# Kernel optimization log

Hardware: AMD Instinct MI355X
Metric: run time of the kernel (lower is better)

## Reference

```python
import jax, jax.numpy as jnp
import numpy as np

D_MODEL, N_HEADS, N_AGENTS = 1024, 16, 64
HEAD_DIM = D_MODEL // N_HEADS
B, N = 4, 4096


def setup_inputs() -> dict:
    key = jax.random.key(0)
    ks = jax.random.split(key, 12)
    hs = HEAD_DIM
    inp = {
        "q": jax.random.normal(ks[0], (B, N_HEADS, N, hs), jnp.float32),
        "k": jax.random.normal(ks[1], (B, N_HEADS, N, hs), jnp.float32),
        "v": jax.random.normal(ks[2], (B, N_HEADS, N, hs), jnp.float32),
        # per-head linear layers (torch nn.Linear: y = x @ W.T + b)
        "Wq": jax.random.normal(ks[3], (hs, hs), jnp.float32) / np.sqrt(hs),
        "bq": jnp.zeros((hs,), jnp.float32),
        "Wk": jax.random.normal(ks[4], (hs, hs), jnp.float32) / np.sqrt(hs),
        "bk": jnp.zeros((hs,), jnp.float32),
        "Wv": jax.random.normal(ks[5], (hs, hs), jnp.float32) / np.sqrt(hs),
        "bv": jnp.zeros((hs,), jnp.float32),
        "Wo": jax.random.normal(ks[6], (D_MODEL, D_MODEL), jnp.float32) / np.sqrt(D_MODEL),
        "bo": jnp.zeros((D_MODEL,), jnp.float32),
        "agent_tokens": jax.random.normal(ks[7], (1, N_HEADS, N_AGENTS, hs), jnp.float32),
    }
    return inp


def reference(q, k, v, Wq, bq, Wk, bk, Wv, bv, Wo, bo, agent_tokens):
    Bq, nh, N_, hs = q.shape
    scale = 1.0 / np.sqrt(hs).astype(np.float32)
    agents = jnp.broadcast_to(agent_tokens, (Bq, nh, N_AGENTS, hs))
    q_agents = jnp.einsum("bhad,ed->bhae", agents, Wq) + bq   # [B,nh,A,hs]
    k_agents = jnp.einsum("bhnd,ed->bhne", k, Wk) + bk        # [B,nh,N,hs]
    v_agents = jnp.einsum("bhnd,ed->bhne", v, Wv) + bv        # [B,nh,N,hs]
    # stage 1: agents attend to keys/values
    scores1 = jnp.einsum("bhad,bhnd->bhan", q_agents, k_agents) * scale
    scores1 = jax.nn.softmax(scores1, axis=-1)
    context1 = jnp.einsum("bhan,bhnd->bhad", scores1, v_agents)  # [B,nh,A,hs]
    # stage 2: queries attend to agent context
    scores2 = jnp.einsum("bhnd,bhad->bhna", q, context1) * scale
    scores2 = jax.nn.softmax(scores2, axis=-1)
    context2 = jnp.einsum("bhna,bhad->bhnd", scores2, context1)  # [B,nh,N,hs]
    context2 = context2.transpose(0, 2, 1, 3).reshape(Bq, N_, nh * hs)
    output = context2 @ Wo.T + bo  # dropout is identity in eval
    return output, scores2
```

## Files before the change

### kernel.cpp

```cpp
#include <hip/hip_runtime.h>

#define NB 4
#define NH 16
#define NN 4096
#define HS 64
#define NA 64
#define DM 1024
#define NBH (NB*NH)
#define SCALE 0.125f

typedef __attribute__((ext_vector_type(8))) short bf16x8;
typedef __attribute__((ext_vector_type(4))) float f32x4;

__device__ __forceinline__ unsigned short f2bf(float f) {
  unsigned u = __float_as_uint(f);
  u += 0x7FFF + ((u >> 16) & 1);
  return (unsigned short)(u >> 16);
}

__device__ __forceinline__ void gload_lds16(const void* g, void* l) {
  __builtin_amdgcn_global_load_lds(
      (const __attribute__((address_space(1))) unsigned int*)g,
      (__attribute__((address_space(3))) unsigned int*)l, 16, 0, 0);
}

__device__ __forceinline__ void fma44(float (&c)[4][4], const float4 a, const float4 b) {
  const float av[4] = {a.x, a.y, a.z, a.w};
  const float bw[4] = {b.x, b.y, b.z, b.w};
#pragma unroll
  for (int i = 0; i < 4; ++i)
#pragma unroll
    for (int j = 0; j < 4; ++j)
      c[i][j] = fmaf(av[i], bw[j], c[i][j]);
}

__device__ __forceinline__ void dot44(float (&c)[4][4], const float4 (&a)[4], const float4 (&b)[4]) {
#pragma unroll
  for (int i = 0; i < 4; ++i)
#pragma unroll
    for (int j = 0; j < 4; ++j) {
      c[i][j] = fmaf(a[i].x, b[j].x, c[i][j]);
      c[i][j] = fmaf(a[i].y, b[j].y, c[i][j]);
      c[i][j] = fmaf(a[i].z, b[j].z, c[i][j]);
      c[i][j] = fmaf(a[i].w, b[j].w, c[i][j]);
    }
}

__global__ __launch_bounds__(256) void k0_fold(
    const float* __restrict__ agents, const float* __restrict__ Wq,
    const float* __restrict__ bq, const float* __restrict__ Wk,
    unsigned short* __restrict__ foldqbf) {
  const int h = blockIdx.x, tid = threadIdx.x;
  const int tn = tid & 15, tm = tid >> 4;
  __shared__ float AG[64][68];
  __shared__ float WB[64][68];
  __shared__ float QA[64][68];
  __shared__ float WKT[64][68];
  for (int i = tid; i < 1024; i += 256) {
    const int r = i >> 4, c4 = (i & 15) * 4;
    *(float4*)&AG[r][c4] = *(const float4*)(agents + h * 4096 + r * 64 + c4);
    *(float4*)&WB[r][c4] = *(const float4*)(Wq + r * 64 + c4);
    const float4 f = *(const float4*)(Wk + r * 64 + c4);
    WKT[c4 + 0][r] = f.x; WKT[c4 + 1][r] = f.y;
    WKT[c4 + 2][r] = f.z; WKT[c4 + 3][r] = f.w;
  }
  __syncthreads();
  {
    const float4 bb = *(const float4*)(bq + tn * 4);
    float acc[4][4];
#pragma unroll
    for (int i = 0; i < 4; ++i) {
      acc[i][0] = bb.x; acc[i][1] = bb.y; acc[i][2] = bb.z; acc[i][3] = bb.w;
    }
    for (int d4 = 0; d4 < 64; d4 += 4) {
      float4 a4[4], b4[4];
#pragma unroll
      for (int i = 0; i < 4; ++i) a4[i] = *(const float4*)&AG[tm * 4 + i][d4];
#pragma unroll
      for (int j = 0; j < 4; ++j) b4[j] = *(const float4*)&WB[tn * 4 + j][d4];
      dot44(acc, a4, b4);
    }
#pragma unroll
    for (int i = 0; i < 4; ++i)
      *(float4*)&QA[tm * 4 + i][tn * 4] =
          make_float4(acc[i][0], acc[i][1], acc[i][2], acc[i][3]);
  }
// ... 76 lines not shown
        kreg[i0] = *(const float4*)(kraw + kvbase + (size_t)(t + 1) * 4096 + (size_t)i * 4);
        vreg[i0] = *(const float4*)(vraw + kvbase + (size_t)(t + 1) * 4096 + (size_t)i * 4);
      }
    }
    __syncthreads();
    const bf16x8 af0 = *(const bf16x8*)&KN[(w * 16 + l15) * 72 + lg * 8];
    const bf16x8 af1 = *(const bf16x8*)&KN[(w * 16 + l15) * 72 + 32 + lg * 8];
    f32x4 sacc[4];
#pragma unroll
    for (int afr = 0; afr < 4; ++afr) {
      sacc[afr] = (f32x4){0.f, 0.f, 0.f, 0.f};
      const bf16x8 b0 = *(const bf16x8*)&FQ[(afr * 16 + l15) * 72 + lg * 8];
      const bf16x8 b1 = *(const bf16x8*)&FQ[(afr * 16 + l15) * 72 + 32 + lg * 8];
      sacc[afr] = __builtin_amdgcn_mfma_f32_16x16x32_bf16(af0, b0, sacc[afr], 0, 0, 0);
      sacc[afr] = __builtin_amdgcn_mfma_f32_16x16x32_bf16(af1, b1, sacc[afr], 0, 0, 0);
    }
#pragma unroll
    for (int afr = 0; afr < 4; ++afr) {
      const unsigned e0 = f2bf(__expf(sacc[afr][0])) | ((unsigned)f2bf(__expf(sacc[afr][1])) << 16);
      const unsigned e1 = f2bf(__expf(sacc[afr][2])) | ((unsigned)f2bf(__expf(sacc[afr][3])) << 16);
      *(uint2*)&ES[(afr * 16 + l15) * 72 + w * 16 + lg * 4] = make_uint2(e0, e1);
    }
    __syncthreads();
    const bf16x8 ea0 = *(const bf16x8*)&ES[(w * 16 + l15) * 72 + lg * 8];
    const bf16x8 ea1 = *(const bf16x8*)&ES[(w * 16 + l15) * 72 + 32 + lg * 8];
    pacc = __builtin_amdgcn_mfma_f32_16x16x32_bf16(ea0, ones, pacc, 0, 0, 0);
    pacc = __builtin_amdgcn_mfma_f32_16x16x32_bf16(ea1, ones, pacc, 0, 0, 0);
#pragma unroll
    for (int df = 0; df < 4; ++df) {
      const int d = df * 16 + l15;
      const int sw = 8 * ((d >> 2) & 7);
      const bf16x8 vb0 = *(const bf16x8*)&VT[d * 72 + ((lg * 8) ^ sw)];
      const bf16x8 vb1 = *(const bf16x8*)&VT[d * 72 + ((32 + lg * 8) ^ sw)];
      ctx[df] = __builtin_amdgcn_mfma_f32_16x16x32_bf16(ea0, vb0, ctx[df], 0, 0, 0);
      ctx[df] = __builtin_amdgcn_mfma_f32_16x16x32_bf16(ea1, vb1, ctx[df], 0, 0, 0);
    }
  }
  const size_t pbase = ((size_t)bh * 16 + chunk) * 4096;
#pragma unroll
  for (int df = 0; df < 4; ++df)
#pragma unroll
    for (int r = 0; r < 4; ++r)
      pctx[pbase + (w * 16 + lg * 4 + r) * 64 + df * 16 + l15] = ctx[df][r];
  if (l15 == 0) {
#pragma unroll
    for (int r = 0; r < 4; ++r)
      psum[((size_t)bh * 16 + chunk) * 64 + w * 16 + lg * 4 + r] = pacc[r];
  }
}

__global__ __launch_bounds__(256) void k3_reduce(
    const float* __restrict__ pctx, const float* __restrict__ psum,
    const float* __restrict__ Wv, const float* __restrict__ bv,
    float* __restrict__ c1n) {
  const int bh = blockIdx.x, tid = threadIdx.x;
  const int tn = tid & 15, tm = tid >> 4;
  __shared__ float sinv[64];
  __shared__ float CT[64][68];
  __shared__ float WT[64][68];
  if (tid < 64) {
    float s = 0.f;
    for (int c = 0; c < 16; ++c) s += psum[((size_t)bh * 16 + c) * 64 + tid];
    sinv[tid] = 1.0f / s;
  }
  for (int i = tid; i < 1024; i += 256) {
    const int e = i >> 4, d4 = (i & 15) * 4;
    const float4 f = *(const float4*)(Wv + e * 64 + d4);
    WT[d4 + 0][e] = f.x; WT[d4 + 1][e] = f.y;
    WT[d4 + 2][e] = f.z; WT[d4 + 3][e] = f.w;
  }
  __syncthreads();
  for (int i4 = tid; i4 < 1024; i4 += 256) {
    const int a = i4 >> 4, d4 = (i4 & 15) * 4;
    float4 s = make_float4(0.f, 0.f, 0.f, 0.f);
    for (int c = 0; c < 16; ++c) {
      const float4 f = *(const float4*)(pctx + ((size_t)bh * 16 + c) * 4096 + a * 64 + d4);
      s.x += f.x; s.y += f.y; s.z += f.z; s.w += f.w;
    }
    const float si = sinv[a];
    CT[d4 + 0][a] = s.x * si; CT[d4 + 1][a] = s.y * si;
    CT[d4 + 2][a] = s.z * si; CT[d4 + 3][a] = s.w * si;
  }
  __syncthreads();
  float acc[4][4];
  const float4 bb = *(const float4*)(bv + tn * 4);
#pragma unroll
  for (int i = 0; i < 4; ++i) {
    acc[i][0] = bb.x; acc[i][1] = bb.y; acc[i][2] = bb.z; acc[i][3] = bb.w;
  }
#pragma unroll 8
  for (int d = 0; d < 64; ++d) {
    const float4 av = *(const float4*)&CT[d][tm * 4];
    const float4 wv = *(const float4*)&WT[d][tn * 4];
    fma44(acc, av, wv);
  }
#pragma unroll
  for (int i = 0; i < 4; ++i)
    *(float4*)(c1n + (size_t)bh * 4096 + (tm * 4 + i) * 64 + tn * 4) =
        make_float4(acc[i][0], acc[i][1], acc[i][2], acc[i][3]);
}

__global__ __launch_bounds__(256) void kG(
    const float* __restrict__ c1n, const float* __restrict__ Wo,
    unsigned short* __restrict__ GT) {
  const int et = blockIdx.x;
  const int bh = blockIdx.y, h = bh & 15;
  const int e0 = et * 256;
  __shared__ unsigned short WoS[256 * 72];
  __shared__ unsigned short C1S[64 * 72];
  const int tid = threadIdx.x;
  const int lane = tid & 63, w = tid >> 6;
  const int l15 = lane & 15, lg = lane >> 4;
  for (int i = tid; i < 4096; i += 256) {
    const int e = i >> 4, d4 = (i & 15) * 4;
    const float4 f = *(const float4*)(Wo + (size_t)(e0 + e) * DM + h * 64 + d4);
    ushort4 o;
    o.x = f2bf(f.x); o.y = f2bf(f.y); o.z = f2bf(f.z); o.w = f2bf(f.w);
    *(ushort4*)&WoS[e * 72 + d4] = o;
  }
  for (int i = tid; i < 1024; i += 256) {
    const int a = i >> 4, d4 = (i & 15) * 4;
    const float4 f = *(const float4*)(c1n + (size_t)bh * 4096 + a * 64 + d4);
    ushort4 o;
    o.x = f2bf(f.x); o.y = f2bf(f.y); o.z = f2bf(f.z); o.w = f2bf(f.w);
    *(ushort4*)&C1S[a * 72 + d4] = o;
  }
  __syncthreads();
  bf16x8 b0[4], b1[4];
#pragma unroll
  for (int at = 0; at < 4; ++at) {
    b0[at] = *(const bf16x8*)&C1S[(at * 16 + l15) * 72 + lg * 8];
    b1[at] = *(const bf16x8*)&C1S[(at * 16 + l15) * 72 + 32 + lg * 8];
  }
#pragma unroll
  for (int et16 = 0; et16 < 4; ++et16) {
    const int erow = w * 64 + et16 * 16 + l15;
    const bf16x8 a0 = *(const bf16x8*)&WoS[erow * 72 + lg * 8];
    const bf16x8 a1 = *(const bf16x8*)&WoS[erow * 72 + 32 + lg * 8];
#pragma unroll
    for (int at = 0; at < 4; ++at) {
      f32x4 acc = (f32x4){0.f, 0.f, 0.f, 0.f};
      acc = __builtin_amdgcn_mfma_f32_16x16x32_bf16(a0, b0[at], acc, 0, 0, 0);
      acc = __builtin_amdgcn_mfma_f32_16x16x32_bf16(a1, b1[at], acc, 0, 0, 0);
      const size_t gbase =
          ((size_t)bh * 1024 + e0 + w * 64 + et16 * 16 + lg * 4) * 64 + at * 16 + l15;
#pragma unroll
      for (int r = 0; r < 4; ++r) GT[gbase + (size_t)r * 64] = f2bf(acc[r]);
    }
  }
}

__global__ __launch_bounds__(256) void k4_mfma(
    const float* __restrict__ q, const float* __restrict__ c1n,
    float* __restrict__ scores2, unsigned short* __restrict__ P2bf) {
  __shared__ unsigned short QN[64 * 72];
  __shared__ unsigned short C1N[64 * 72];
  __shared__ unsigned short PS[64 * 72];
  const int bh = blockIdx.y;
  const int n0 = blockIdx.x * 64;
  const int tid = threadIdx.x;
  const int lane = tid & 63, w = tid >> 6;
  const int l15 = lane & 15, lg = lane >> 4;

  for (int i = tid; i < 1024; i += 256) {
    const int r = i >> 4, c4 = (i & 15) * 4;
    const float4 f = *(const float4*)(q + ((size_t)bh * NN + n0 + r) * HS + c4);
    *(uint2*)&QN[r * 72 + c4] = make_uint2(
        f2bf(f.x * SCALE) | ((unsigned)f2bf(f.y * SCALE) << 16),
        f2bf(f.z * SCALE) | ((unsigned)f2bf(f.w * SCALE) << 16));
    const float4 g = *(const float4*)(c1n + (size_t)bh * 4096 + r * 64 + c4);
    *(uint2*)&C1N[r * 72 + c4] = make_uint2(
        f2bf(g.x) | ((unsigned)f2bf(g.y) << 16),
        f2bf(g.z) | ((unsigned)f2bf(g.w) << 16));
  }
  __syncthreads();
  const bf16x8 af0 = *(const bf16x8*)&QN[(w * 16 + l15) * 72 + lg * 8];
  const bf16x8 af1 = *(const bf16x8*)&QN[(w * 16 + l15) * 72 + 32 + lg * 8];
  f32x4 sacc[4];
#pragma unroll
  for (int afr = 0; afr < 4; ++afr) {
    sacc[afr] = (f32x4){0.f, 0.f, 0.f, 0.f};
    const bf16x8 b0 = *(const bf16x8*)&C1N[(afr * 16 + l15) * 72 + lg * 8];
    const bf16x8 b1 = *(const bf16x8*)&C1N[(afr * 16 + l15) * 72 + 32 + lg * 8];
    sacc[afr] = __builtin_amdgcn_mfma_f32_16x16x32_bf16(af0, b0, sacc[afr], 0, 0, 0);
    sacc[afr] = __builtin_amdgcn_mfma_f32_16x16x32_bf16(af1, b1, sacc[afr], 0, 0, 0);
  }
  float p[4][4];
#pragma unroll
  for (int r = 0; r < 4; ++r) {
    float m = fmaxf(fmaxf(sacc[0][r], sacc[1][r]), fmaxf(sacc[2][r], sacc[3][r]));
#pragma unroll
    for (int off = 1; off < 16; off <<= 1) m = fmaxf(m, __shfl_xor(m, off));
    float s = 0.f;
#pragma unroll
    for (int afr = 0; afr < 4; ++afr) {
      p[afr][r] = __expf(sacc[afr][r] - m);
      s += p[afr][r];
    }
#pragma unroll
    for (int off = 1; off < 16; off <<= 1) s += __shfl_xor(s, off);
    const float inv = 1.0f / s;
    const size_t srow = ((size_t)bh * NN + n0 + w * 16 + lg * 4 + r) * NA;
#pragma unroll
    for (int afr = 0; afr < 4; ++afr) {
      p[afr][r] *= inv;
      scores2[srow + afr * 16 + l15] = p[afr][r];
      PS[(w * 16 + lg * 4 + r) * 72 + afr * 16 + l15] = f2bf(p[afr][r]);
    }
  }
  const int prow = w * 16 + (lane >> 2);
  const int pch = (lane & 3) * 16;
  const uint4 v0 = *(const uint4*)&PS[prow * 72 + pch];
  const uint4 v1 = *(const uint4*)&PS[prow * 72 + pch + 8];
  unsigned short* gp = P2bf + ((size_t)bh * NN + n0 + prow) * NA + pch;
  *(uint4*)gp = v0;
  *(uint4*)(gp + 8) = v1;
}

__global__ __launch_bounds__(512, 1) void k5_mfma(
    const unsigned short* __restrict__ P2, const unsigned short* __restrict__ GT,
    const float* __restrict__ bo, float* __restrict__ out) {
  __shared__ unsigned short As[2][256 * 64];
  __shared__ unsigned short Bs[2][256 * 64];
  const int tid = threadIdx.x;
  const int lane = tid & 63;
  const int w = tid >> 6;
  const int wr = w >> 2, wc = w & 3;
  const int l15 = lane & 15, lg = lane >> 4;
  const int mblk = blockIdx.x;
  const int b16 = (mblk >> 4) * 16;
  const int nloc0 = (mblk & 15) * 256;
  const int e0 = blockIdx.y * 256;

  const int srow8 = lane >> 3;
  const int sslot = ((lane & 7) ^ srow8) << 4;

  f32x4 acc[8][4] = {{{0.f}}};

#define K5_STAGE(T, BUF)                                                       \
  {                                                                            \
    const char* Ab = (const char*)(P2 + ((size_t)(b16 + (T)) * NN + nloc0) * NA); \
    const char* Gb = (const char*)(GT + ((size_t)(b16 + (T)) * 1024 + e0) * NA);  \
    _Pragma("unroll")                                                          \
    for (int j = 0; j < 4; ++j) {                                              \
      const int rb = j * 64 + w * 8;                \
      const int r = rb + srow8;                                                \
      gload_lds16(Ab + (size_t)r * 128 + sslot,                                \
                  (char*)As[BUF] + rb * 128 + lane * 16);                      \
      gload_lds16(Gb + (size_t)r * 128 + sslot,                                \
                  (char*)Bs[BUF] + rb * 128 + lane * 16);                      \
    }                                                                          \
  }

  K5_STAGE(0, 0);
  K5_STAGE(1, 1);
  for (int t = 0; t < 16; ++t) {
    if (t < 15) {
      asm volatile("s_waitcnt vmcnt(8)" ::: "memory");
    } else {
      asm volatile("s_waitcnt vmcnt(0)" ::: "memory");
    }
    __builtin_amdgcn_sched_barrier(0);
    __builtin_amdgcn_s_barrier();
    __builtin_amdgcn_sched_barrier(0);
    const char* Ac = (const char*)As[t & 1];
    const char* Bc = (const char*)Bs[t & 1];
#pragma unroll
    for (int ks = 0; ks < 2; ++ks) {
      bf16x8 af[8], bfr[4];
#pragma unroll
      for (int m = 0; m < 8; ++m) {
        const int r = wr * 128 + m * 16 + l15;
        const int byt = (ks * 64 + lg * 16) ^ ((r & 7) << 4);
        af[m] = *(const bf16x8*)(Ac + r * 128 + byt);
      }
#pragma unroll
      for (int n = 0; n < 4; ++n) {
        const int r = wc * 64 + n * 16 + l15;
        const int byt = (ks * 64 + lg * 16) ^ ((r & 7) << 4);
        bfr[n] = *(const bf16x8*)(Bc + r * 128 + byt);
      }
#pragma unroll
      for (int m = 0; m < 8; ++m)
#pragma unroll
        for (int n = 0; n < 4; ++n)
          acc[m][n] = __builtin_amdgcn_mfma_f32_16x16x32_bf16(af[m], bfr[n], acc[m][n], 0, 0, 0);
    }
    __builtin_amdgcn_sched_barrier(0);
    __builtin_amdgcn_s_barrier();
    __builtin_amdgcn_sched_barrier(0);
    if (t + 2 < 16) K5_STAGE(t + 2, t & 1);
  }
#undef K5_STAGE

  const size_t mrow0 = (size_t)(b16 >> 4) * NN + nloc0;
#pragma unroll
  for (int m = 0; m < 8; ++m) {
    const size_t row0 = mrow0 + wr * 128 + m * 16 + lg * 4;
#pragma unroll
    for (int n = 0; n < 4; ++n) {
      const int c = e0 + wc * 64 + n * 16 + l15;
      const float bias = bo[c];
#pragma unroll
      for (int r = 0; r < 4; ++r)
        out[(row0 + r) * DM + c] = acc[m][n][r] + bias;
    }
  }
}

extern "C" void kernel_launch(void* const* d_in, const int* in_sizes, int n_in,
                              void* d_out, int out_size, void* d_ws, size_t ws_size,
                              hipStream_t stream) {
  (void)in_sizes; (void)n_in; (void)out_size; (void)ws_size;
  const float* q  = (const float*)d_in[0];
  const float* k  = (const float*)d_in[1];
  const float* v  = (const float*)d_in[2];
  const float* Wq = (const float*)d_in[3];
  const float* bq = (const float*)d_in[4];
  const float* Wk = (const float*)d_in[5];
  const float* bk = (const float*)d_in[6];
  const float* Wv = (const float*)d_in[7];
  const float* bv = (const float*)d_in[8];
  const float* Wo = (const float*)d_in[9];
  const float* bo = (const float*)d_in[10];
  const float* ag = (const float*)d_in[11];
  (void)bk;

  float* out0 = (float*)d_out;
  float* scores2 = out0 + (size_t)NB * NN * DM;

  float* ws = (float*)d_ws;
  unsigned short* foldqbf = (unsigned short*)ws;
  float* c1n = ws + 65536;
  float* psum = c1n + 262144;
  float* pctx = psum + 65536;
  unsigned short* GT = (unsigned short*)pctx;
  unsigned short* P2bf = (unsigned short*)(pctx + 4194304);

  k0_fold<<<NH, 256, 0, stream>>>(ag, Wq, bq, Wk, foldqbf);
  k2_mfma<<<dim3(16, NBH), 256, 0, stream>>>(k, v, foldqbf, pctx, psum);
  k3_reduce<<<NBH, 256, 0, stream>>>(pctx, psum, Wv, bv, c1n);
  kG<<<dim3(4, NBH), 256, 0, stream>>>(c1n, Wo, GT);
  k4_mfma<<<dim3(NN / 64, NBH), 256, 0, stream>>>(q, c1n, scores2, P2bf);
  k5_mfma<<<dim3(NB * NN / 256, DM / 256), 512, 0, stream>>>(P2bf, GT, bo, out0);
}
```

Measured before the change: 152.5 us.

## Interleave k5 prefetch with MFMA quadrants, swizzle blocks, split k3 reduce

The k5 GEMM main loop is restructured into four MFMA quadrants per K-step. Each quadrant loads only its own LDS fragments, interleaves one quarter of the next tile's global-to-LDS loads, and raises wave priority with s_setprio around the MFMA bursts. The block index is swizzled so neighbouring workgroups share P2/GT tiles in cache. k3_reduce is split into 4 blocks per head over the agent dimension to get more parallelism, at the cost of reloading Wv per block. The added barriers and the single-buffer-ahead prefetch risk extra sync overhead.

```diff
diff --git a/kernel.cpp b/kernel.cpp
--- a/kernel.cpp
+++ b/kernel.cpp
@@ -215,14 +215,17 @@
     const float* __restrict__ pctx, const float* __restrict__ psum,
     const float* __restrict__ Wv, const float* __restrict__ bv,
     float* __restrict__ c1n) {
-  const int bh = blockIdx.x, tid = threadIdx.x;
+  const int bh = blockIdx.x, aq = blockIdx.y;
+  const int tid = threadIdx.x;
   const int tn = tid & 15, tm = tid >> 4;
-  __shared__ float sinv[64];
-  __shared__ float CT[64][68];
+  __shared__ float sinv[16];
+  __shared__ float CR[16][68];
   __shared__ float WT[64][68];
-  if (tid < 64) {
+  if (tid < 16) {
+    const int a = aq * 16 + tid;
     float s = 0.f;
-    for (int c = 0; c < 16; ++c) s += psum[((size_t)bh * 16 + c) * 64 + tid];
+#pragma unroll 4
+    for (int c = 0; c < 16; ++c) s += psum[((size_t)bh * 16 + c) * 64 + a];
     sinv[tid] = 1.0f / s;
   }
   for (int i = tid; i < 1024; i += 256) {
@@ -232,34 +235,34 @@
     WT[d4 + 2][e] = f.z; WT[d4 + 3][e] = f.w;
   }
   __syncthreads();
-  for (int i4 = tid; i4 < 1024; i4 += 256) {
-    const int a = i4 >> 4, d4 = (i4 & 15) * 4;
+  {
+    const int al = tid >> 4, d4 = (tid & 15) * 4;
+    const size_t base = (size_t)bh * 16 * 4096 + (size_t)(aq * 16 + al) * 64 + d4;
     float4 s = make_float4(0.f, 0.f, 0.f, 0.f);
+#pragma unroll 4
     for (int c = 0; c < 16; ++c) {
-      const float4 f = *(const float4*)(pctx + ((size_t)bh * 16 + c) * 4096 + a * 64 + d4);
+      const float4 f = *(const float4*)(pctx + base + (size_t)c * 4096);
       s.x += f.x; s.y += f.y; s.z += f.z; s.w += f.w;
     }
-    const float si = sinv[a];
-    CT[d4 + 0][a] = s.x * si; CT[d4 + 1][a] = s.y * si;
-    CT[d4 + 2][a] = s.z * si; CT[d4 + 3][a] = s.w * si;
+    const float si = sinv[al];
+    CR[al][d4 + 0] = s.x * si; CR[al][d4 + 1] = s.y * si;
+    CR[al][d4 + 2] = s.z * si; CR[al][d4 + 3] = s.w * si;
   }
   __syncthreads();
-  float acc[4][4];
+  float acc[4];
   const float4 bb = *(const float4*)(bv + tn * 4);
-#pragma unroll
-  for (int i = 0; i < 4; ++i) {
-    acc[i][0] = bb.x; acc[i][1] = bb.y; acc[i][2] = bb.z; acc[i][3] = bb.w;
-  }
+  acc[0] = bb.x; acc[1] = bb.y; acc[2] = bb.z; acc[3] = bb.w;
 #pragma unroll 8
   for (int d = 0; d < 64; ++d) {
-    const float4 av = *(const float4*)&CT[d][tm * 4];
-    const float4 wv = *(const float4*)&WT[d][tn * 4];
-    fma44(acc, av, wv);
-  }
-#pragma unroll
-  for (int i = 0; i < 4; ++i)
-    *(float4*)(c1n + (size_t)bh * 4096 + (tm * 4 + i) * 64 + tn * 4) =
-        make_float4(acc[i][0], acc[i][1], acc[i][2], acc[i][3]);
+    const float a0 = CR[tm][d];
+    const float4 wv4 = *(const float4*)&WT[d][tn * 4];
+    acc[0] = fmaf(a0, wv4.x, acc[0]);
+    acc[1] = fmaf(a0, wv4.y, acc[1]);
+    acc[2] = fmaf(a0, wv4.z, acc[2]);
+    acc[3] = fmaf(a0, wv4.w, acc[3]);
+  }
+  *(float4*)(c1n + (size_t)bh * 4096 + (size_t)(aq * 16 + tm) * 64 + tn * 4) =
+      make_float4(acc[0], acc[1], acc[2], acc[3]);
 }
 
 __global__ __launch_bounds__(256) void kG(
@@ -389,71 +392,114 @@
   const int w = tid >> 6;
   const int wr = w >> 2, wc = w & 3;
   const int l15 = lane & 15, lg = lane >> 4;
-  const int mblk = blockIdx.x;
+  const int fid = blockIdx.x + 64 * blockIdx.y;
+  const int swz = (fid & 7) * 32 + (fid >> 3);
+  const int mblk = swz & 63;
+  const int e0 = (swz >> 6) * 256;
   const int b16 = (mblk >> 4) * 16;
   const int nloc0 = (mblk & 15) * 256;
-  const int e0 = blockIdx.y * 256;
 
   const int srow8 = lane >> 3;
   const int sslot = ((lane & 7) ^ srow8) << 4;
 
   f32x4 acc[8][4] = {{{0.f}}};
 
-#define K5_STAGE(T, BUF)                                                       \
-  {                                                                            \
-    const char* Ab = (const char*)(P2 + ((size_t)(b16 + (T)) * NN + nloc0) * NA); \
-    const char* Gb = (const char*)(GT + ((size_t)(b16 + (T)) * 1024 + e0) * NA);  \
-    _Pragma("unroll")                                                          \
-    for (int j = 0; j < 4; ++j) {                                              \
-      const int rb = j * 64 + w * 8;                \
-      const int r = rb + srow8;                                                \
-      gload_lds16(Ab + (size_t)r * 128 + sslot,                                \
-                  (char*)As[BUF] + rb * 128 + lane * 16);                      \
-      gload_lds16(Gb + (size_t)r * 128 + sslot,                                \
-                  (char*)Bs[BUF] + rb * 128 + lane * 16);                      \
-    }                                                                          \
-  }
-
-  K5_STAGE(0, 0);
-  K5_STAGE(1, 1);
+#define K5_STAGE_PART(T, J, BUF)                                                 \
+  {                                                                              \
+    const char* Ab = (const char*)(P2 + ((size_t)(b16 + (T)) * NN + nloc0) * NA);\
+    const char* Gb = (const char*)(GT + ((size_t)(b16 + (T)) * 1024 + e0) * NA); \
+    const int rb = (J) * 64 + w * 8;                  \
+    const int r = rb + srow8;                                                    \
+    gload_lds16(Ab + (size_t)r * 128 + sslot,                                    \
+                (char*)As[BUF] + rb * 128 + lane * 16);                          \
+    gload_lds16(Gb + (size_t)r * 128 + sslot,                                    \
+                (char*)Bs[BUF] + rb * 128 + lane * 16);                          \
+  }
+
+#define K5_LOAD_AF(MH)                                                  \
+  _Pragma("unroll") for (int m = 0; m < 4; ++m) {                       \
+    const int r = wr * 128 + (MH) * 64 + m * 16 + l15;                  \
+    _Pragma("unroll") for (int ks = 0; ks < 2; ++ks) {                  \
+      const int byt = (ks * 64 + lg * 16) ^ ((r & 7) << 4);             \
+      af[m][ks] = *(const bf16x8*)(Ac + r * 128 + byt);                 \
+    }                                                                   \
+  }
+
+#define K5_LOAD_BF(NH2)                                                 \
+  _Pragma("unroll") for (int n = 0; n < 2; ++n) {                       \
+    const int r = wc * 64 + (NH2) * 32 + n * 16 + l15;                  \
+    _Pragma("unroll") for (int ks = 0; ks < 2; ++ks) {                  \
+      const int byt = (ks * 64 + lg * 16) ^ ((r & 7) << 4);             \
+      bfv[n][ks] = *(const bf16x8*)(Bc + r * 128 + byt);                \
+    }                                                                   \
+  }
+
+#define K5_MFMA_Q(MH, NH2)                                                       \
+  _Pragma("unroll") for (int ks = 0; ks < 2; ++ks)                               \
+  _Pragma("unroll") for (int m = 0; m < 4; ++m)                                  \
+  _Pragma("unroll") for (int n = 0; n < 2; ++n)                                  \
+    acc[(MH) * 4 + m][(NH2) * 2 + n] = __builtin_amdgcn_mfma_f32_16x16x32_bf16(  \
+        af[m][ks], bfv[n][ks], acc[(MH) * 4 + m][(NH2) * 2 + n], 0, 0, 0);
+
+#define K5_BAR()                        \
+  __builtin_amdgcn_sched_barrier(0);    \
+  __builtin_amdgcn_s_barrier();         \
+  __builtin_amdgcn_sched_barrier(0);
+
+  K5_STAGE_PART(0, 0, 0);
+  K5_STAGE_PART(0, 1, 0);
+  K5_STAGE_PART(0, 2, 0);
+  K5_STAGE_PART(0, 3, 0);
+
   for (int t = 0; t < 16; ++t) {
+    const char* Ac = (const char*)As[t & 1];
+    const char* Bc = (const char*)Bs[t & 1];
+    const int nb = (t + 1) & 1;
+    bf16x8 af[4][2], bfv[2][2];
+
     if (t < 15) {
-      asm volatile("s_waitcnt vmcnt(8)" ::: "memory");
+      K5_STAGE_PART(t + 1, 0, nb);
+      asm volatile("s_waitcnt vmcnt(2)" ::: "memory");
     } else {
       asm volatile("s_waitcnt vmcnt(0)" ::: "memory");
     }
-    __builtin_amdgcn_sched_barrier(0);
-    __builtin_amdgcn_s_barrier();
-    __builtin_amdgcn_sched_barrier(0);
-    const char* Ac = (const char*)As[t & 1];
-    const char* Bc = (const char*)Bs[t & 1];
-#pragma unroll
-    for (int ks = 0; ks < 2; ++ks) {
-      bf16x8 af[8], bfr[4];
-#pragma unroll
-      for (int m = 0; m < 8; ++m) {
-        const int r = wr * 128 + m * 16 + l15;
-        const int byt = (ks * 64 + lg * 16) ^ ((r & 7) << 4);
-        af[m] = *(const bf16x8*)(Ac + r * 128 + byt);
-      }
-#pragma unroll
-      for (int n = 0; n < 4; ++n) {
-        const int r = wc * 64 + n * 16 + l15;
-        const int byt = (ks * 64 + lg * 16) ^ ((r & 7) << 4);
-        bfr[n] = *(const bf16x8*)(Bc + r * 128 + byt);
-      }
-#pragma unroll
-      for (int m = 0; m < 8; ++m)
-#pragma unroll
-        for (int n = 0; n < 4; ++n)
-          acc[m][n] = __builtin_amdgcn_mfma_f32_16x16x32_bf16(af[m], bfr[n], acc[m][n], 0, 0, 0);
-    }
-    __builtin_amdgcn_sched_barrier(0);
-    __builtin_amdgcn_s_barrier();
-    __builtin_amdgcn_sched_barrier(0);
-    if (t + 2 < 16) K5_STAGE(t + 2, t & 1);
-  }
-#undef K5_STAGE
+    K5_BAR();
+    K5_LOAD_AF(0);
+    K5_LOAD_BF(0);
+    __builtin_amdgcn_s_setprio(1);
+    K5_MFMA_Q(0, 0);
+    __builtin_amdgcn_s_setprio(0);
+    K5_BAR();
+
+    K5_LOAD_BF(1);
+    if (t < 15) K5_STAGE_PART(t + 1, 1, nb);
+    K5_BAR();
+    __builtin_amdgcn_s_setprio(1);
+    K5_MFMA_Q(0, 1);
+    __builtin_amdgcn_s_setprio(0);
+    K5_BAR();
+
+    K5_LOAD_AF(1);
+    if (t < 15) K5_STAGE_PART(t + 1, 2, nb);
+    K5_BAR();
+    __builtin_amdgcn_s_setprio(1);
+    K5_MFMA_Q(1, 1);
+    __builtin_amdgcn_s_setprio(0);
+    K5_BAR();
+
+    K5_LOAD_BF(0);
+    if (t < 15) K5_STAGE_PART(t + 1, 3, nb);
+    K5_BAR();
+    __builtin_amdgcn_s_setprio(1);
+    K5_MFMA_Q(1, 0);
+    __builtin_amdgcn_s_setprio(0);
+    K5_BAR();
+  }
+#undef K5_BAR
+#undef K5_MFMA_Q
+#undef K5_LOAD_BF
+#undef K5_LOAD_AF
+#undef K5_STAGE_PART
 
   const size_t mrow0 = (size_t)(b16 >> 4) * NN + nloc0;
 #pragma unroll
@@ -501,7 +547,7 @@
 
   k0_fold<<<NH, 256, 0, stream>>>(ag, Wq, bq, Wk, foldqbf);
   k2_mfma<<<dim3(16, NBH), 256, 0, stream>>>(k, v, foldqbf, pctx, psum);
-  k3_reduce<<<NBH, 256, 0, stream>>>(pctx, psum, Wv, bv, c1n);
+  k3_reduce<<<dim3(NBH, 4), 256, 0, stream>>>(pctx, psum, Wv, bv, c1n);
   kG<<<dim3(4, NBH), 256, 0, stream>>>(c1n, Wo, GT);
   k4_mfma<<<dim3(NN / 64, NBH), 256, 0, stream>>>(q, c1n, scores2, P2bf);
   k5_mfma<<<dim3(NB * NN / 256, DM / 256), 512, 0, stream>>>(P2bf, GT, bo, out0);
```

Measured after the change: 155.6 us. 2.0% more time.

## Fuse stage-2 softmax with output projection and store context in bf16

Applied to the files above, without the earlier changes.

Merges the stage-2 score/softmax kernel and the output projection GEMM into one kernel. Each block owns 64 rows of one batch and loops over head pairs, building bf16 probabilities in LDS and feeding them straight into MFMA against GT, so the P2 intermediate is never written to or read back from global memory. The reduce kernel now splits across four agent quarters and emits bf16 context, which removes repeated conversions downstream. The fused kernel launches only 256 blocks of 512 threads and reads GT directly from global memory without LDS staging or double buffering, so occupancy and load latency may suffer.

```diff
diff --git a/kernel.cpp b/kernel.cpp
--- a/kernel.cpp
+++ b/kernel.cpp
@@ -16,22 +16,6 @@
   unsigned u = __float_as_uint(f);
   u += 0x7FFF + ((u >> 16) & 1);
   return (unsigned short)(u >> 16);
-}
-
-__device__ __forceinline__ void gload_lds16(const void* g, void* l) {
-  __builtin_amdgcn_global_load_lds(
-      (const __attribute__((address_space(1))) unsigned int*)g,
-      (__attribute__((address_space(3))) unsigned int*)l, 16, 0, 0);
-}
-
-__device__ __forceinline__ void fma44(float (&c)[4][4], const float4 a, const float4 b) {
-  const float av[4] = {a.x, a.y, a.z, a.w};
-  const float bw[4] = {b.x, b.y, b.z, b.w};
-#pragma unroll
-  for (int i = 0; i < 4; ++i)
-#pragma unroll
-    for (int j = 0; j < 4; ++j)
-      c[i][j] = fmaf(av[i], bw[j], c[i][j]);
 }
 
 __device__ __forceinline__ void dot44(float (&c)[4][4], const float4 (&a)[4], const float4 (&b)[4]) {
@@ -214,15 +198,18 @@
 __global__ __launch_bounds__(256) void k3_reduce(
     const float* __restrict__ pctx, const float* __restrict__ psum,
     const float* __restrict__ Wv, const float* __restrict__ bv,
-    float* __restrict__ c1n) {
-  const int bh = blockIdx.x, tid = threadIdx.x;
+    unsigned short* __restrict__ c1nbf) {
+  const int bh = blockIdx.x, aq = blockIdx.y;
+  const int tid = threadIdx.x;
   const int tn = tid & 15, tm = tid >> 4;
-  __shared__ float sinv[64];
-  __shared__ float CT[64][68];
+  __shared__ float sinv[16];
+  __shared__ float CR[16][68];
   __shared__ float WT[64][68];
-  if (tid < 64) {
+  if (tid < 16) {
+    const int a = aq * 16 + tid;
     float s = 0.f;
-    for (int c = 0; c < 16; ++c) s += psum[((size_t)bh * 16 + c) * 64 + tid];
+#pragma unroll 4
+    for (int c = 0; c < 16; ++c) s += psum[((size_t)bh * 16 + c) * 64 + a];
     sinv[tid] = 1.0f / s;
   }
   for (int i = tid; i < 1024; i += 256) {
@@ -232,38 +219,39 @@
     WT[d4 + 2][e] = f.z; WT[d4 + 3][e] = f.w;
   }
   __syncthreads();
-  for (int i4 = tid; i4 < 1024; i4 += 256) {
-    const int a = i4 >> 4, d4 = (i4 & 15) * 4;
+  {
+    const int al = tid >> 4, d4 = (tid & 15) * 4;
+    const size_t base = (size_t)bh * 16 * 4096 + (size_t)(aq * 16 + al) * 64 + d4;
     float4 s = make_float4(0.f, 0.f, 0.f, 0.f);
+#pragma unroll 4
     for (int c = 0; c < 16; ++c) {
-      const float4 f = *(const float4*)(pctx + ((size_t)bh * 16 + c) * 4096 + a * 64 + d4);
+      const float4 f = *(const float4*)(pctx + base + (size_t)c * 4096);
       s.x += f.x; s.y += f.y; s.z += f.z; s.w += f.w;
     }
-    const float si = sinv[a];
-    CT[d4 + 0][a] = s.x * si; CT[d4 + 1][a] = s.y * si;
-    CT[d4 + 2][a] = s.z * si; CT[d4 + 3][a] = s.w * si;
+    const float si = sinv[al];
+    CR[al][d4 + 0] = s.x * si; CR[al][d4 + 1] = s.y * si;
+    CR[al][d4 + 2] = s.z * si; CR[al][d4 + 3] = s.w * si;
   }
   __syncthreads();
-  float acc[4][4];
+  float acc[4];
   const float4 bb = *(const float4*)(bv + tn * 4);
-#pragma unroll
-  for (int i = 0; i < 4; ++i) {
-    acc[i][0] = bb.x; acc[i][1] = bb.y; acc[i][2] = bb.z; acc[i][3] = bb.w;
-  }
+  acc[0] = bb.x; acc[1] = bb.y; acc[2] = bb.z; acc[3] = bb.w;
 #pragma unroll 8
   for (int d = 0; d < 64; ++d) {
-    const float4 av = *(const float4*)&CT[d][tm * 4];
-    const float4 wv = *(const float4*)&WT[d][tn * 4];
-    fma44(acc, av, wv);
-  }
-#pragma unroll
-  for (int i = 0; i < 4; ++i)
-    *(float4*)(c1n + (size_t)bh * 4096 + (tm * 4 + i) * 64 + tn * 4) =
-        make_float4(acc[i][0], acc[i][1], acc[i][2], acc[i][3]);
+    const float a0 = CR[tm][d];
+    const float4 wv4 = *(const float4*)&WT[d][tn * 4];
+    acc[0] = fmaf(a0, wv4.x, acc[0]);
+    acc[1] = fmaf(a0, wv4.y, acc[1]);
+    acc[2] = fmaf(a0, wv4.z, acc[2]);
+    acc[3] = fmaf(a0, wv4.w, acc[3]);
+  }
+  ushort4 o;
+  o.x = f2bf(acc[0]); o.y = f2bf(acc[1]); o.z = f2bf(acc[2]); o.w = f2bf(acc[3]);
+  *(ushort4*)(c1nbf + (size_t)bh * 4096 + (size_t)(aq * 16 + tm) * 64 + tn * 4) = o;
 }
 
 __global__ __launch_bounds__(256) void kG(
-    const float* __restrict__ c1n, const float* __restrict__ Wo,
+    const unsigned short* __restrict__ c1nbf, const float* __restrict__ Wo,
     unsigned short* __restrict__ GT) {
   const int et = blockIdx.x;
   const int bh = blockIdx.y, h = bh & 15;
@@ -280,12 +268,10 @@
     o.x = f2bf(f.x); o.y = f2bf(f.y); o.z = f2bf(f.z); o.w = f2bf(f.w);
     *(ushort4*)&WoS[e * 72 + d4] = o;
   }
-  for (int i = tid; i < 1024; i += 256) {
-    const int a = i >> 4, d4 = (i & 15) * 4;
-    const float4 f = *(const float4*)(c1n + (size_t)bh * 4096 + a * 64 + d4);
-    ushort4 o;
-    o.x = f2bf(f.x); o.y = f2bf(f.y); o.z = f2bf(f.z); o.w = f2bf(f.w);
-    *(ushort4*)&C1S[a * 72 + d4] = o;
+  for (int i = tid; i < 512; i += 256) {
+    const int a = i >> 3, d8 = (i & 7) * 8;
+    *(uint4*)&C1S[a * 72 + d8] =
+        *(const uint4*)(c1nbf + (size_t)bh * 4096 + a * 64 + d8);
   }
   __syncthreads();
   bf16x8 b0[4], b1[4];
@@ -312,160 +298,132 @@
   }
 }
 
-__global__ __launch_bounds__(256) void k4_mfma(
-    const float* __restrict__ q, const float* __restrict__ c1n,
-    float* __restrict__ scores2, unsigned short* __restrict__ P2bf) {
-  __shared__ unsigned short QN[64 * 72];
-  __shared__ unsigned short C1N[64 * 72];
-  __shared__ unsigned short PS[64 * 72];
-  const int bh = blockIdx.y;
-  const int n0 = blockIdx.x * 64;
+__global__ __launch_bounds__(512, 1) void k45_fused(
+    const float* __restrict__ q, const unsigned short* __restrict__ c1nbf,
+    const unsigned short* __restrict__ GT, const float* __restrict__ bo,
+    float* __restrict__ scores2, float* __restrict__ out) {
+  __shared__ unsigned short QN[2][64 * 72];
+  __shared__ unsigned short C1N[2][64 * 72];
+  __shared__ unsigned short PS[2][64 * 72];
   const int tid = threadIdx.x;
   const int lane = tid & 63, w = tid >> 6;
   const int l15 = lane & 15, lg = lane >> 4;
-
-  for (int i = tid; i < 1024; i += 256) {
-    const int r = i >> 4, c4 = (i & 15) * 4;
-    const float4 f = *(const float4*)(q + ((size_t)bh * NN + n0 + r) * HS + c4);
-    *(uint2*)&QN[r * 72 + c4] = make_uint2(
-        f2bf(f.x * SCALE) | ((unsigned)f2bf(f.y * SCALE) << 16),
-        f2bf(f.z * SCALE) | ((unsigned)f2bf(f.w * SCALE) << 16));
-    const float4 g = *(const float4*)(c1n + (size_t)bh * 4096 + r * 64 + c4);
-    *(uint2*)&C1N[r * 72 + c4] = make_uint2(
-        f2bf(g.x) | ((unsigned)f2bf(g.y) << 16),
-        f2bf(g.z) | ((unsigned)f2bf(g.w) << 16));
-  }
-  __syncthreads();
-  const bf16x8 af0 = *(const bf16x8*)&QN[(w * 16 + l15) * 72 + lg * 8];
-  const bf16x8 af1 = *(const bf16x8*)&QN[(w * 16 + l15) * 72 + 32 + lg * 8];
-  f32x4 sacc[4];
-#pragma unroll
-  for (int afr = 0; afr < 4; ++afr) {
-    sacc[afr] = (f32x4){0.f, 0.f, 0.f, 0.f};
-    const bf16x8 b0 = *(const bf16x8*)&C1N[(afr * 16 + l15) * 72 + lg * 8];
-    const bf16x8 b1 = *(const bf16x8*)&C1N[(afr * 16 + l15) * 72 + 32 + lg * 8];
-    sacc[afr] = __builtin_amdgcn_mfma_f32_16x16x32_bf16(af0, b0, sacc[afr], 0, 0, 0);
-    sacc[afr] = __builtin_amdgcn_mfma_f32_16x16x32_bf16(af1, b1, sacc[afr], 0, 0, 0);
-  }
-  float p[4][4];
-#pragma unroll
-  for (int r = 0; r < 4; ++r) {
-    float m = fmaxf(fmaxf(sacc[0][r], sacc[1][r]), fmaxf(sacc[2][r], sacc[3][r]));
-#pragma unroll
-    for (int off = 1; off < 16; off <<= 1) m = fmaxf(m, __shfl_xor(m, off));
-    float s = 0.f;
+  const int phys = blockIdx.x;
+  const int r8 = phys & 7;
+  const int b = r8 >> 1;
+  const int n0 = ((r8 & 1) + 2 * (phys >> 3)) * 64;
+
+  const int sr = tid >> 3, sd8 = (tid & 7) * 8;
+
+  float4 sq[2][2];
+
+#define K45_LOADQ(H0)                                                           \
+  _Pragma("unroll") for (int it = 0; it < 2; ++it) {                            \
+    const size_t qb = ((size_t)(b * 16 + (H0) + it) * NN + n0 + sr) * 64 + sd8; \
+    sq[it][0] = *(const float4*)(q + qb);                                       \
+    sq[it][1] = *(const float4*)(q + qb + 4);                                   \
+  }
+
+#define K45_STOREQC(H0)                                                         \
+  _Pragma("unroll") for (int it = 0; it < 2; ++it) {                            \
+    uint4 o;                                                                    \
+    o.x = f2bf(sq[it][0].x * SCALE) | ((unsigned)f2bf(sq[it][0].y * SCALE) << 16); \
+    o.y = f2bf(sq[it][0].z * SCALE) | ((unsigned)f2bf(sq[it][0].w * SCALE) << 16); \
+    o.z = f2bf(sq[it][1].x * SCALE) | ((unsigned)f2bf(sq[it][1].y * SCALE) << 16); \
+    o.w = f2bf(sq[it][1].z * SCALE) | ((unsigned)f2bf(sq[it][1].w * SCALE) << 16); \
+    *(uint4*)&QN[it][sr * 72 + sd8] = o;                                        \
+    *(uint4*)&C1N[it][sr * 72 + sd8] = *(const uint4*)(                         \
+        c1nbf + (size_t)(b * 16 + (H0) + it) * 4096 + sr * 64 + sd8);           \
+  }
+
+  f32x4 acc[4][8];
+#pragma unroll
+  for (int mf = 0; mf < 4; ++mf)
+#pragma unroll
+    for (int nf = 0; nf < 8; ++nf) acc[mf][nf] = (f32x4){0.f, 0.f, 0.f, 0.f};
+
+  K45_LOADQ(0);
+
+  const int hh_q = w >> 2;
+  const int rq = (w & 3) * 16;
+
+  for (int hp = 0; hp < 8; ++hp) {
+    const int h0 = hp * 2;
+    __syncthreads();
+    K45_STOREQC(h0);
+    if (hp < 7) K45_LOADQ(h0 + 2);
+    __syncthreads();
+    const bf16x8 a0 = *(const bf16x8*)&QN[hh_q][(rq + l15) * 72 + lg * 8];
+    const bf16x8 a1 = *(const bf16x8*)&QN[hh_q][(rq + l15) * 72 + 32 + lg * 8];
+    f32x4 sacc[4];
 #pragma unroll
     for (int afr = 0; afr < 4; ++afr) {
-      p[afr][r] = __expf(sacc[afr][r] - m);
-      s += p[afr][r];
-    }
-#pragma unroll
-    for (int off = 1; off < 16; off <<= 1) s += __shfl_xor(s, off);
-    const float inv = 1.0f / s;
-    const size_t srow = ((size_t)bh * NN + n0 + w * 16 + lg * 4 + r) * NA;
-#pragma unroll
-    for (int afr = 0; afr < 4; ++afr) {
-      p[afr][r] *= inv;
-      scores2[srow + afr * 16 + l15] = p[afr][r];
-      PS[(w * 16 + lg * 4 + r) * 72 + afr * 16 + l15] = f2bf(p[afr][r]);
-    }
-  }
-  const int prow = w * 16 + (lane >> 2);
-  const int pch = (lane & 3) * 16;
-  const uint4 v0 = *(const uint4*)&PS[prow * 72 + pch];
-  const uint4 v1 = *(const uint4*)&PS[prow * 72 + pch + 8];
-  unsigned short* gp = P2bf + ((size_t)bh * NN + n0 + prow) * NA + pch;
-  *(uint4*)gp = v0;
-  *(uint4*)(gp + 8) = v1;
-}
-
-__global__ __launch_bounds__(512, 1) void k5_mfma(
-    const unsigned short* __restrict__ P2, const unsigned short* __restrict__ GT,
-    const float* __restrict__ bo, float* __restrict__ out) {
-  __shared__ unsigned short As[2][256 * 64];
-  __shared__ unsigned short Bs[2][256 * 64];
-  const int tid = threadIdx.x;
-  const int lane = tid & 63;
-  const int w = tid >> 6;
-  const int wr = w >> 2, wc = w & 3;
-  const int l15 = lane & 15, lg = lane >> 4;
-  const int mblk = blockIdx.x;
-  const int b16 = (mblk >> 4) * 16;
-  const int nloc0 = (mblk & 15) * 256;
-  const int e0 = blockIdx.y * 256;
-
-  const int srow8 = lane >> 3;
-  const int sslot = ((lane & 7) ^ srow8) << 4;
-
-  f32x4 acc[8][4] = {{{0.f}}};
-
-#define K5_STAGE(T, BUF)                                                       \
-  {                                                                            \
-    const char* Ab = (const char*)(P2 + ((size_t)(b16 + (T)) * NN + nloc0) * NA); \
-    const char* Gb = (const char*)(GT + ((size_t)(b16 + (T)) * 1024 + e0) * NA);  \
-    _Pragma("unroll")                                                          \
-    for (int j = 0; j < 4; ++j) {                                              \
-      const int rb = j * 64 + w * 8;                \
-      const int r = rb + srow8;                                                \
-      gload_lds16(Ab + (size_t)r * 128 + sslot,                                \
-                  (char*)As[BUF] + rb * 128 + lane * 16);                      \
-      gload_lds16(Gb + (size_t)r * 128 + sslot,                                \
-                  (char*)Bs[BUF] + rb * 128 + lane * 16);                      \
-    }                                                                          \
-  }
-
-  K5_STAGE(0, 0);
-  K5_STAGE(1, 1);
-  for (int t = 0; t < 16; ++t) {
-    if (t < 15) {
-      asm volatile("s_waitcnt vmcnt(8)" ::: "memory");
-    } else {
-      asm volatile("s_waitcnt vmcnt(0)" ::: "memory");
-    }
-    __builtin_amdgcn_sched_barrier(0);
-    __builtin_amdgcn_s_barrier();
-    __builtin_amdgcn_sched_barrier(0);
-    const char* Ac = (const char*)As[t & 1];
-    const char* Bc = (const char*)Bs[t & 1];
-#pragma unroll
-    for (int ks = 0; ks < 2; ++ks) {
-      bf16x8 af[8], bfr[4];
-#pragma unroll
-      for (int m = 0; m < 8; ++m) {
-        const int r = wr * 128 + m * 16 + l15;
-        const int byt = (ks * 64 + lg * 16) ^ ((r & 7) << 4);
-        af[m] = *(const bf16x8*)(Ac + r * 128 + byt);
+      sacc[afr] = (f32x4){0.f, 0.f, 0.f, 0.f};
+      const bf16x8 b0 = *(const bf16x8*)&C1N[hh_q][(afr * 16 + l15) * 72 + lg * 8];
+      const bf16x8 b1 = *(const bf16x8*)&C1N[hh_q][(afr * 16 + l15) * 72 + 32 + lg * 8];
+      sacc[afr] = __builtin_amdgcn_mfma_f32_16x16x32_bf16(a0, b0, sacc[afr], 0, 0, 0);
+      sacc[afr] = __builtin_amdgcn_mfma_f32_16x16x32_bf16(a1, b1, sacc[afr], 0, 0, 0);
+    }
+    const int bh_q = b * 16 + h0 + hh_q;
+#pragma unroll
+    for (int r = 0; r < 4; ++r) {
+      float m = fmaxf(fmaxf(sacc[0][r], sacc[1][r]), fmaxf(sacc[2][r], sacc[3][r]));
+#pragma unroll
+      for (int off = 1; off < 16; off <<= 1) m = fmaxf(m, __shfl_xor(m, off));
+      float p[4];
+      float s = 0.f;
+#pragma unroll
+      for (int afr = 0; afr < 4; ++afr) {
+        p[afr] = __expf(sacc[afr][r] - m);
+        s += p[afr];
       }
 #pragma unroll
-      for (int n = 0; n < 4; ++n) {
-        const int r = wc * 64 + n * 16 + l15;
-        const int byt = (ks * 64 + lg * 16) ^ ((r & 7) << 4);
-        bfr[n] = *(const bf16x8*)(Bc + r * 128 + byt);
+      for (int off = 1; off < 16; off <<= 1) s += __shfl_xor(s, off);
+      const float inv = 1.0f / s;
+      const size_t srow = ((size_t)bh_q * NN + n0 + rq + lg * 4 + r) * NA;
+#pragma unroll
+      for (int afr = 0; afr < 4; ++afr) {
+        const float pv = p[afr] * inv;
+        scores2[srow + afr * 16 + l15] = pv;
+        PS[hh_q][(rq + lg * 4 + r) * 72 + afr * 16 + l15] = f2bf(pv);
       }
-#pragma unroll
-      for (int m = 0; m < 8; ++m)
-#pragma unroll
-        for (int n = 0; n < 4; ++n)
-          acc[m][n] = __builtin_amdgcn_mfma_f32_16x16x32_bf16(af[m], bfr[n], acc[m][n], 0, 0, 0);
-    }
-    __builtin_amdgcn_sched_barrier(0);
-    __builtin_amdgcn_s_barrier();
-    __builtin_amdgcn_sched_barrier(0);
-    if (t + 2 < 16) K5_STAGE(t + 2, t & 1);
-  }
-#undef K5_STAGE
-
-  const size_t mrow0 = (size_t)(b16 >> 4) * NN + nloc0;
-#pragma unroll
-  for (int m = 0; m < 8; ++m) {
-    const size_t row0 = mrow0 + wr * 128 + m * 16 + lg * 4;
-#pragma unroll
-    for (int n = 0; n < 4; ++n) {
-      const int c = e0 + wc * 64 + n * 16 + l15;
-      const float bias = bo[c];
+    }
+    __syncthreads();
+#pragma unroll
+    for (int hh = 0; hh < 2; ++hh) {
+      const unsigned short* gtb =
+          GT + ((size_t)(b * 16 + h0 + hh) * 1024 + w * 128) * 64;
+#pragma unroll
+      for (int ks = 0; ks < 2; ++ks) {
+        bf16x8 bfv[8];
+#pragma unroll
+        for (int nf = 0; nf < 8; ++nf)
+          bfv[nf] = *(const bf16x8*)(gtb + (nf * 16 + l15) * 64 + ks * 32 + lg * 8);
+#pragma unroll
+        for (int mf = 0; mf < 4; ++mf) {
+          const bf16x8 af =
+              *(const bf16x8*)&PS[hh][(mf * 16 + l15) * 72 + ks * 32 + lg * 8];
+#pragma unroll
+          for (int nf = 0; nf < 8; ++nf)
+            acc[mf][nf] = __builtin_amdgcn_mfma_f32_16x16x32_bf16(
+                af, bfv[nf], acc[mf][nf], 0, 0, 0);
+        }
+      }
+    }
+  }
+#undef K45_LOADQ
+#undef K45_STOREQC
+
+#pragma unroll
+  for (int nf = 0; nf < 8; ++nf) {
+    const int col = w * 128 + nf * 16 + l15;
+    const float bias = bo[col];
+#pragma unroll
+    for (int mf = 0; mf < 4; ++mf) {
+      const size_t row0 = (size_t)b * NN + n0 + mf * 16 + lg * 4;
 #pragma unroll
       for (int r = 0; r < 4; ++r)
-        out[(row0 + r) * DM + c] = acc[m][n][r] + bias;
+        out[(row0 + r) * DM + col] = acc[mf][nf][r] + bias;
     }
   }
 }
@@ -493,16 +451,14 @@
 
   float* ws = (float*)d_ws;
   unsigned short* foldqbf = (unsigned short*)ws;
-  float* c1n = ws + 65536;
-  float* psum = c1n + 262144;
+  unsigned short* c1nbf = (unsigned short*)(ws + 65536);
+  float* psum = ws + 65536 + 262144;
   float* pctx = psum + 65536;
   unsigned short* GT = (unsigned short*)pctx;
-  unsigned short* P2bf = (unsigned short*)(pctx + 4194304);
 
   k0_fold<<<NH, 256, 0, stream>>>(ag, Wq, bq, Wk, foldqbf);
   k2_mfma<<<dim3(16, NBH), 256, 0, stream>>>(k, v, foldqbf, pctx, psum);
-  k3_reduce<<<NBH, 256, 0, stream>>>(pctx, psum, Wv, bv, c1n);
-  kG<<<dim3(4, NBH), 256, 0, stream>>>(c1n, Wo, GT);
-  k4_mfma<<<dim3(NN / 64, NBH), 256, 0, stream>>>(q, c1n, scores2, P2bf);
-  k5_mfma<<<dim3(NB * NN / 256, DM / 256), 512, 0, stream>>>(P2bf, GT, bo, out0);
-}
+  k3_reduce<<<dim3(NBH, 4), 256, 0, stream>>>(pctx, psum, Wv, bv, c1nbf);
+  kG<<<dim3(4, NBH), 256, 0, stream>>>(c1nbf, Wo, GT);
+  k45_fused<<<256, 512, 0, stream>>>(q, c1nbf, GT, bo, scores2, out0);
+}
```

Result: slower. 177.5 us (+16.4%).

## Split context reduction across agent quarters, store bf16 context, load q directly

Applied to the files above, without the earlier changes.

k3_reduce is parallelised over four agent quarters and writes context1 as bf16. Downstream kG and k4 then copy bf16 rows directly rather than converting fp32. k4 also builds its q MFMA fragments straight from global loads into registers, skipping LDS staging. The aim is more parallelism in the reduce, less conversion and traffic, and less LDS use. The trade-offs are Wv being reloaded per block and a less coalesced q access pattern.

```diff
diff --git a/kernel.cpp b/kernel.cpp
--- a/kernel.cpp
+++ b/kernel.cpp
@@ -22,16 +22,6 @@
   __builtin_amdgcn_global_load_lds(
       (const __attribute__((address_space(1))) unsigned int*)g,
       (__attribute__((address_space(3))) unsigned int*)l, 16, 0, 0);
-}
-
-__device__ __forceinline__ void fma44(float (&c)[4][4], const float4 a, const float4 b) {
-  const float av[4] = {a.x, a.y, a.z, a.w};
-  const float bw[4] = {b.x, b.y, b.z, b.w};
-#pragma unroll
-  for (int i = 0; i < 4; ++i)
-#pragma unroll
-    for (int j = 0; j < 4; ++j)
-      c[i][j] = fmaf(av[i], bw[j], c[i][j]);
 }
 
 __device__ __forceinline__ void dot44(float (&c)[4][4], const float4 (&a)[4], const float4 (&b)[4]) {
@@ -214,15 +204,18 @@
 __global__ __launch_bounds__(256) void k3_reduce(
     const float* __restrict__ pctx, const float* __restrict__ psum,
     const float* __restrict__ Wv, const float* __restrict__ bv,
-    float* __restrict__ c1n) {
-  const int bh = blockIdx.x, tid = threadIdx.x;
+    unsigned short* __restrict__ c1nbf) {
+  const int bh = blockIdx.x, aq = blockIdx.y;
+  const int tid = threadIdx.x;
   const int tn = tid & 15, tm = tid >> 4;
-  __shared__ float sinv[64];
-  __shared__ float CT[64][68];
+  __shared__ float sinv[16];
+  __shared__ float CR[16][68];
   __shared__ float WT[64][68];
-  if (tid < 64) {
+  if (tid < 16) {
+    const int a = aq * 16 + tid;
     float s = 0.f;
-    for (int c = 0; c < 16; ++c) s += psum[((size_t)bh * 16 + c) * 64 + tid];
+#pragma unroll 4
+    for (int c = 0; c < 16; ++c) s += psum[((size_t)bh * 16 + c) * 64 + a];
     sinv[tid] = 1.0f / s;
   }
   for (int i = tid; i < 1024; i += 256) {
@@ -232,38 +225,39 @@
     WT[d4 + 2][e] = f.z; WT[d4 + 3][e] = f.w;
   }
   __syncthreads();
-  for (int i4 = tid; i4 < 1024; i4 += 256) {
-    const int a = i4 >> 4, d4 = (i4 & 15) * 4;
+  {
+    const int al = tid >> 4, d4 = (tid & 15) * 4;
+    const size_t base = (size_t)bh * 16 * 4096 + (size_t)(aq * 16 + al) * 64 + d4;
     float4 s = make_float4(0.f, 0.f, 0.f, 0.f);
+#pragma unroll 4
     for (int c = 0; c < 16; ++c) {
-      const float4 f = *(const float4*)(pctx + ((size_t)bh * 16 + c) * 4096 + a * 64 + d4);
+      const float4 f = *(const float4*)(pctx + base + (size_t)c * 4096);
       s.x += f.x; s.y += f.y; s.z += f.z; s.w += f.w;
     }
-    const float si = sinv[a];
-    CT[d4 + 0][a] = s.x * si; CT[d4 + 1][a] = s.y * si;
-    CT[d4 + 2][a] = s.z * si; CT[d4 + 3][a] = s.w * si;
+    const float si = sinv[al];
+    CR[al][d4 + 0] = s.x * si; CR[al][d4 + 1] = s.y * si;
+    CR[al][d4 + 2] = s.z * si; CR[al][d4 + 3] = s.w * si;
   }
   __syncthreads();
-  float acc[4][4];
+  float acc[4];
   const float4 bb = *(const float4*)(bv + tn * 4);
-#pragma unroll
-  for (int i = 0; i < 4; ++i) {
-    acc[i][0] = bb.x; acc[i][1] = bb.y; acc[i][2] = bb.z; acc[i][3] = bb.w;
-  }
+  acc[0] = bb.x; acc[1] = bb.y; acc[2] = bb.z; acc[3] = bb.w;
 #pragma unroll 8
   for (int d = 0; d < 64; ++d) {
-    const float4 av = *(const float4*)&CT[d][tm * 4];
-    const float4 wv = *(const float4*)&WT[d][tn * 4];
-    fma44(acc, av, wv);
-  }
-#pragma unroll
-  for (int i = 0; i < 4; ++i)
-    *(float4*)(c1n + (size_t)bh * 4096 + (tm * 4 + i) * 64 + tn * 4) =
-        make_float4(acc[i][0], acc[i][1], acc[i][2], acc[i][3]);
+    const float a0 = CR[tm][d];
+    const float4 wv4 = *(const float4*)&WT[d][tn * 4];
+    acc[0] = fmaf(a0, wv4.x, acc[0]);
+    acc[1] = fmaf(a0, wv4.y, acc[1]);
+    acc[2] = fmaf(a0, wv4.z, acc[2]);
+    acc[3] = fmaf(a0, wv4.w, acc[3]);
+  }
+  ushort4 o;
+  o.x = f2bf(acc[0]); o.y = f2bf(acc[1]); o.z = f2bf(acc[2]); o.w = f2bf(acc[3]);
+  *(ushort4*)(c1nbf + (size_t)bh * 4096 + (size_t)(aq * 16 + tm) * 64 + tn * 4) = o;
 }
 
 __global__ __launch_bounds__(256) void kG(
-    const float* __restrict__ c1n, const float* __restrict__ Wo,
+    const unsigned short* __restrict__ c1nbf, const float* __restrict__ Wo,
     unsigned short* __restrict__ GT) {
   const int et = blockIdx.x;
   const int bh = blockIdx.y, h = bh & 15;
@@ -280,12 +274,10 @@
     o.x = f2bf(f.x); o.y = f2bf(f.y); o.z = f2bf(f.z); o.w = f2bf(f.w);
     *(ushort4*)&WoS[e * 72 + d4] = o;
   }
-  for (int i = tid; i < 1024; i += 256) {
-    const int a = i >> 4, d4 = (i & 15) * 4;
-    const float4 f = *(const float4*)(c1n + (size_t)bh * 4096 + a * 64 + d4);
-    ushort4 o;
-    o.x = f2bf(f.x); o.y = f2bf(f.y); o.z = f2bf(f.z); o.w = f2bf(f.w);
-    *(ushort4*)&C1S[a * 72 + d4] = o;
+  for (int i = tid; i < 512; i += 256) {
+    const int a = i >> 3, d8 = (i & 7) * 8;
+    *(uint4*)&C1S[a * 72 + d8] =
+        *(const uint4*)(c1nbf + (size_t)bh * 4096 + a * 64 + d8);
   }
   __syncthreads();
   bf16x8 b0[4], b1[4];
@@ -313,9 +305,8 @@
 }
 
 __global__ __launch_bounds__(256) void k4_mfma(
-    const float* __restrict__ q, const float* __restrict__ c1n,
+    const float* __restrict__ q, const unsigned short* __restrict__ c1nbf,
     float* __restrict__ scores2, unsigned short* __restrict__ P2bf) {
-  __shared__ unsigned short QN[64 * 72];
   __shared__ unsigned short C1N[64 * 72];
   __shared__ unsigned short PS[64 * 72];
   const int bh = blockIdx.y;
@@ -324,20 +315,27 @@
   const int lane = tid & 63, w = tid >> 6;
   const int l15 = lane & 15, lg = lane >> 4;
 
-  for (int i = tid; i < 1024; i += 256) {
-    const int r = i >> 4, c4 = (i & 15) * 4;
-    const float4 f = *(const float4*)(q + ((size_t)bh * NN + n0 + r) * HS + c4);
-    *(uint2*)&QN[r * 72 + c4] = make_uint2(
-        f2bf(f.x * SCALE) | ((unsigned)f2bf(f.y * SCALE) << 16),
-        f2bf(f.z * SCALE) | ((unsigned)f2bf(f.w * SCALE) << 16));
-    const float4 g = *(const float4*)(c1n + (size_t)bh * 4096 + r * 64 + c4);
-    *(uint2*)&C1N[r * 72 + c4] = make_uint2(
-        f2bf(g.x) | ((unsigned)f2bf(g.y) << 16),
-        f2bf(g.z) | ((unsigned)f2bf(g.w) << 16));
-  }
+  for (int i = tid; i < 512; i += 256) {
+    const int a = i >> 3, d8 = (i & 7) * 8;
+    *(uint4*)&C1N[a * 72 + d8] =
+        *(const uint4*)(c1nbf + (size_t)bh * 4096 + a * 64 + d8);
+  }
+  const float* qr = q + ((size_t)bh * NN + n0 + w * 16 + l15) * HS;
+  const float4 qa = *(const float4*)(qr + lg * 8);
+  const float4 qb = *(const float4*)(qr + lg * 8 + 4);
+  const float4 qc = *(const float4*)(qr + 32 + lg * 8);
+  const float4 qd = *(const float4*)(qr + 32 + lg * 8 + 4);
+  bf16x8 af0, af1;
+  af0[0] = (short)f2bf(qa.x * SCALE); af0[1] = (short)f2bf(qa.y * SCALE);
+  af0[2] = (short)f2bf(qa.z * SCALE); af0[3] = (short)f2bf(qa.w * SCALE);
+  af0[4] = (short)f2bf(qb.x * SCALE); af0[5] = (short)f2bf(qb.y * SCALE);
+  af0[6] = (short)f2bf(qb.z * SCALE); af0[7] = (short)f2bf(qb.w * SCALE);
+  af1[0] = (short)f2bf(qc.x * SCALE); af1[1] = (short)f2bf(qc.y * SCALE);
+  af1[2] = (short)f2bf(qc.z * SCALE); af1[3] = (short)f2bf(qc.w * SCALE);
+  af1[4] = (short)f2bf(qd.x * SCALE); af1[5] = (short)f2bf(qd.y * SCALE);
+  af1[6] = (short)f2bf(qd.z * SCALE); af1[7] = (short)f2bf(qd.w * SCALE);
   __syncthreads();
-  const bf16x8 af0 = *(const bf16x8*)&QN[(w * 16 + l15) * 72 + lg * 8];
-  const bf16x8 af1 = *(const bf16x8*)&QN[(w * 16 + l15) * 72 + 32 + lg * 8];
+
   f32x4 sacc[4];
 #pragma unroll
   for (int afr = 0; afr < 4; ++afr) {
@@ -493,16 +491,16 @@
 
   float* ws = (float*)d_ws;
   unsigned short* foldqbf = (unsigned short*)ws;
-  float* c1n = ws + 65536;
-  float* psum = c1n + 262144;
+  unsigned short* c1nbf = (unsigned short*)(ws + 65536);
+  float* psum = ws + 65536 + 262144;
   float* pctx = psum + 65536;
   unsigned short* GT = (unsigned short*)pctx;
   unsigned short* P2bf = (unsigned short*)(pctx + 4194304);
 
   k0_fold<<<NH, 256, 0, stream>>>(ag, Wq, bq, Wk, foldqbf);
   k2_mfma<<<dim3(16, NBH), 256, 0, stream>>>(k, v, foldqbf, pctx, psum);
-  k3_reduce<<<NBH, 256, 0, stream>>>(pctx, psum, Wv, bv, c1n);
-  kG<<<dim3(4, NBH), 256, 0, stream>>>(c1n, Wo, GT);
-  k4_mfma<<<dim3(NN / 64, NBH), 256, 0, stream>>>(q, c1n, scores2, P2bf);
+  k3_reduce<<<dim3(NBH, 4), 256, 0, stream>>>(pctx, psum, Wv, bv, c1nbf);
+  kG<<<dim3(4, NBH), 256, 0, stream>>>(c1nbf, Wo, GT);
+  k4_mfma<<<dim3(NN / 64, NBH), 256, 0, stream>>>(q, c1nbf, scores2, P2bf);
   k5_mfma<<<dim3(NB * NN / 256, DM / 256), 512, 0, stream>>>(P2bf, GT, bo, out0);
 }
```

Result: faster. 145.4 us (-4.6%).
